# Optimization experiments

Measured on AMD Instinct MI355X. Metric: run time of the kernel, lower is better.

## Reference

```python
import jax, jax.numpy as jnp
import numpy as np

N = 100000
IN_CH = 500
H = 8           # heads
C1 = 8          # conv1 out_channels per head -> hidden 64
NCLS = 3        # conv2 out_channels (concat=False -> mean over heads)
NEG_SLOPE = 0.2


def _gatv2_layer(x, src, dst, Wl, Wr, att, bias, heads, ch, concat):
    n = x.shape[0]
    xl = (x @ Wl).reshape(n, heads, ch)   # source transform
    xr = (x @ Wr).reshape(n, heads, ch)   # target transform
    # per-edge attention logits: a^T LeakyReLU(xl[j] + xr[i])
    e = jax.nn.leaky_relu(xl[src] + xr[dst], NEG_SLOPE)   # [E,H,C]
    logits = jnp.einsum('ehc,hc->eh', e, att)             # [E,H]
    # segment softmax over edges sharing the same destination node
    m = jax.ops.segment_max(logits, dst, num_segments=n)  # [N,H]
    ex = jnp.exp(logits - m[dst])
    denom = jax.ops.segment_sum(ex, dst, num_segments=n)  # [N,H]
    alpha = ex / denom[dst]                               # [E,H]
    # scatter-add aggregation of source features weighted by attention
    out = jax.ops.segment_sum(alpha[:, :, None] * xl[src], dst, num_segments=n)  # [N,H,C]
    out = out.reshape(n, heads * ch) if concat else out.mean(axis=1)
    return out + bias


def _add_self_loops(edge_index, n):
    loop = jnp.arange(n, dtype=edge_index.dtype)
    src = jnp.concatenate([edge_index[0], loop])
    dst = jnp.concatenate([edge_index[1], loop])
    return src, dst


def setup_inputs() -> dict:
    key = jax.random.key(0)
    ks = jax.random.split(key, 10)
    E = 1600000
    x = jax.random.normal(ks[0], (N, IN_CH), dtype=jnp.float32)
    edge_index = jax.random.randint(ks[1], (2, E), 0, N, dtype=jnp.int64)
    s1 = 1.0 / np.sqrt(IN_CH)
    s2 = 1.0 / np.sqrt(H * C1)
    return {
        'x': x,
        'edge_index': edge_index,
        'W1l': jax.random.normal(ks[2], (IN_CH, H * C1), dtype=jnp.float32) * s1,
        'W1r': jax.random.normal(ks[3], (IN_CH, H * C1), dtype=jnp.float32) * s1,
        'att1': jax.random.normal(ks[4], (H, C1), dtype=jnp.float32) * 0.3,
        'b1': jnp.zeros((H * C1,), dtype=jnp.float32),
        'W2l': jax.random.normal(ks[5], (H * C1, H * NCLS), dtype=jnp.float32) * s2,
        'W2r': jax.random.normal(ks[6], (H * C1, H * NCLS), dtype=jnp.float32) * s2,
        'att2': jax.random.normal(ks[7], (H, NCLS), dtype=jnp.float32) * 0.3,
        'b2': jnp.zeros((NCLS,), dtype=jnp.float32),
    }


def reference(x, edge_index, W1l, W1r, att1, b1, W2l, W2r, att2, b2):
    # eval mode: dropout(p=0.6) is identity
    src, dst = _add_self_loops(edge_index, x.shape[0])
    h = _gatv2_layer(x, src, dst, W1l, W1r, att1, b1, H, C1, concat=True)
    h = jax.nn.elu(h)
    h = _gatv2_layer(h, src, dst, W2l, W2r, att2, b2, H, NCLS, concat=False)
    return jax.nn.softmax(h, axis=1)
```

## Files before the change

### kernel.cpp

```cpp
#include <hip/hip_runtime.h>
#include <cstdint>
#include <cstddef>

#define N_NODES 100000
#define E_EDGES 1600000
#define E_TOT   1700000
#define HEADS   8
#define C1      8
#define HC1     64
#define NCLS    3
#define HC2     24
#define IN_CH   500
#define NEG     0.2f

#define TILES   6250
#define NBLK    256

#define NPB     391
#define NBUCK   256
#define CHUNK   4096
#define NCHUNK  416
#define SCAP    8192

typedef __attribute__((ext_vector_type(8))) _Float16 f16x8;
typedef __attribute__((ext_vector_type(4))) _Float16 f16x4;
typedef __attribute__((ext_vector_type(4))) float f32x4;

__device__ __forceinline__ int edge_at(const int* __restrict__ ei, int idx, int mode) {
  return mode ? ei[idx] : ei[2 * idx];
}

__device__ __forceinline__ int detect_mode(const int* __restrict__ ei,
                                           int tid, int* shflag) {
  if (tid == 0) *shflag = 0;
  __syncthreads();
  int nz = 0;
#pragma unroll
  for (int i = 0; i < 16; ++i) nz |= ei[2 * (i * 256 + tid) + 1];
  if (__ballot(nz != 0)) {
    if ((tid & 63) == 0) atomicOr(shflag, 1);
  }
  __syncthreads();
  return *shflag;
}


__global__ __launch_bounds__(256) void k_cntA(const int* __restrict__ ei,
    int* __restrict__ cmat, const float* __restrict__ W1l,
    const float* __restrict__ W1r, _Float16* __restrict__ Wimg) {
  __shared__ int cnt[NBUCK];
  __shared__ int shflag;
  const int tid = threadIdx.x;

  if (blockIdx.x >= NCHUNK) {
    int b2 = blockIdx.x - NCHUNK;
    int t = b2 * 256 + tid;
    int col = t >> 9, k = t & 511;
    float v = 0.f;
    if (k < IN_CH) v = (col < HC1) ? W1l[k * HC1 + col] : W1r[k * HC1 + (col - HC1)];
    int boff = (col * 1024 + k * 2) ^ ((col & 7) << 4);
    Wimg[boff >> 1] = (_Float16)v;
    return;
  }

  const int mode = detect_mode(ei, tid, &shflag);
  const int e0 = blockIdx.x * CHUNK;
  cnt[tid] = 0;
  __syncthreads();
#pragma unroll
  for (int i = 0; i < 16; ++i) {
    int e = e0 + i * 256 + tid;
    if (e < E_TOT) {
      int d = (e < E_EDGES) ? edge_at(ei, E_EDGES + e, mode) : (e - E_EDGES);
      atomicAdd(&cnt[d / NPB], 1);
    }
  }
  __syncthreads();
  cmat[blockIdx.x * NBUCK + tid] = cnt[tid];
}

__global__ void k_scanA(int* __restrict__ cmat, int* __restrict__ bbase,
                        int* __restrict__ rowptr) {
  __shared__ int sh[NBUCK];
  int b = threadIdx.x;
  int run = 0;
  for (int c = 0; c < NCHUNK; ++c) {
    int v = cmat[c * NBUCK + b];
    cmat[c * NBUCK + b] = run;
    run += v;
  }
  int tot = run;
  sh[b] = tot;
  __syncthreads();
  for (int off = 1; off < NBUCK; off <<= 1) {
    int add = (b >= off) ? sh[b - off] : 0;
    __syncthreads();
    sh[b] += add;
    __syncthreads();
  }
  bbase[b] = sh[b] - tot;
  if (b == NBUCK - 1) {
    bbase[NBUCK] = sh[b];
    rowptr[N_NODES] = sh[b];
  }
}

__global__ __launch_bounds__(256) void k_grpA(const int* __restrict__ ei,
    const int* __restrict__ cmat, const int* __restrict__ bbase,
    unsigned* __restrict__ bstage) {
  __shared__ int cnt[NBUCK], ofs[NBUCK], cur[NBUCK], gbase[NBUCK];
  __shared__ unsigned buf[CHUNK];
  __shared__ int shflag;
  const int tid = threadIdx.x;
  const int e0 = blockIdx.x * CHUNK;
  const int mode = detect_mode(ei, tid, &shflag);
  cnt[tid] = 0;
  __syncthreads();

  unsigned pk[16]; int bk[16];
#pragma unroll
  for (int i = 0; i < 16; ++i) {
    int e = e0 + i * 256 + tid;
    bk[i] = -1;
    if (e < E_TOT) {
      int s, d;
      if (e < E_EDGES) { s = edge_at(ei, e, mode); d = edge_at(ei, E_EDGES + e, mode); }
      else             { s = e - E_EDGES; d = s; }
      int b = d / NPB;
      bk[i] = b;
      pk[i] = ((unsigned)s << 9) | (unsigned)(d - b * NPB);
      atomicAdd(&cnt[b], 1);
    }
  }
  __syncthreads();
  ofs[tid] = cnt[tid];
  __syncthreads();
  for (int off = 1; off < NBUCK; off <<= 1) {
    int add = (tid >= off) ? ofs[tid - off] : 0;
    __syncthreads();
    ofs[tid] += add;
    __syncthreads();
  }
  ofs[tid] -= cnt[tid];
  cur[tid] = ofs[tid];
  gbase[tid] = bbase[tid] + cmat[blockIdx.x * NBUCK + tid];
  __syncthreads();
#pragma unroll
  for (int i = 0; i < 16; ++i) {
    if (bk[i] >= 0) {
      int slot = atomicAdd(&cur[bk[i]], 1);
      buf[slot] = pk[i];
    }
  }
  __syncthreads();
  const int n = cnt[tid], s0 = ofs[tid], g = gbase[tid];
  for (int j = 0; j < n; ++j) {
    int gp = g + j;
    if ((unsigned)gp < (unsigned)E_TOT) bstage[gp] = buf[s0 + j];
  }
}

__global__ __launch_bounds__(256) void k_partB(const unsigned* __restrict__ bstage,
    const int* __restrict__ bbase, int* __restrict__ rowptr, int* __restrict__ esrc) {
  __shared__ unsigned edges[SCAP];
  __shared__ int lhist[NPB + 1];
  __shared__ int lptr[NPB];
  __shared__ int sh[256];
  const int b = blockIdx.x;
  const int tid = threadIdx.x;
  const int base = bbase[b];
  const int n = min(bbase[b + 1] - base, SCAP);
  const int nl = min(NPB, N_NODES - b * NPB);

  for (int k = tid; k < NPB; k += 256) lhist[k] = 0;
  for (int i = tid; i < n; i += 256) edges[i] = bstage[base + i];
  __syncthreads();
  for (int i = tid; i < n; i += 256) atomicAdd(&lhist[(int)(edges[i] & 511u)], 1);
  __syncthreads();
  int i0 = tid * 2;
  int v0 = (i0 < nl) ? lhist[i0] : 0;
  int v1 = (i0 + 1 < nl) ? lhist[i0 + 1] : 0;
  int tsum = v0 + v1;
  sh[tid] = tsum;
  __syncthreads();
  for (int off = 1; off < 256; off <<= 1) {
    int add = (tid >= off) ? sh[tid - off] : 0;
    __syncthreads();
    sh[tid] += add;
    __syncthreads();
  }
  int run = base + sh[tid] - tsum;
  if (i0 < nl)     lptr[i0] = run;
  if (i0 + 1 < nl) lptr[i0 + 1] = run + v0;
  __syncthreads();
  for (int k = tid; k < nl; k += 256) rowptr[b * NPB + k] = lptr[k];
  __syncthreads();
  for (int i = tid; i < n; i += 256) {
    unsigned pkv = edges[i];
    int pos = atomicAdd(&lptr[(int)(pkv & 511u)], 1);
    if ((unsigned)pos < (unsigned)E_TOT) esrc[pos] = (int)(pkv >> 9);
  }
}

#define ALO   16384
#define PBASE 32768

__global__ __launch_bounds__(512, 1) void k_gemm1(const float* __restrict__ x,
    const _Float16* __restrict__ Wimg, _Float16* __restrict__ xlh,
    float* __restrict__ xr) {
  __shared__ char lds[40960];
  const int tid  = threadIdx.x;
  const int lane = tid & 63, wid = tid >> 6;
  const int lrow = lane & 15, kg = lane >> 4;
  const int colgrp = wid & 3;
  const int kw0 = (wid >> 2) * 8;

  f16x8 bf[2][8];
#pragma unroll
  for (int n = 0; n < 2; ++n) {
    int col = colgrp * 32 + n * 16 + lrow;
#pragma unroll
    for (int kw = 0; kw < 8; ++kw) {
      int koff = (kw0 + kw) * 64 + kg * 16;
      int bo = (col * 1024 + koff) ^ ((col & 7) << 4);
      bf[n][kw] = *(const f16x8*)((const char*)Wimg + bo);
    }
  }

  int xoff[4], aoff[4], mode[4];
#pragma unroll
  for (int i = 0; i < 4; ++i) {
    int s = tid + i * 512;
    if (s < 2000) {
      int row = s / 125, c4 = s - row * 125;
      xoff[i] = row * 500 + c4 * 4;
      aoff[i] = (row * 1024 + c4 * 8) ^ ((row & 7) << 4);
      mode[i] = 0;
    } else {
      int p = s - 2000;
      int row = p / 3, j = p - row * 3;
      aoff[i] = (row * 1024 + 1000 + j * 8) ^ ((row & 7) << 4);
      xoff[i] = 0;
      mode[i] = 1;
    }
  }

  float4 rv[4];
  auto loadregs = [&](int tile) {
#pragma unroll
    for (int i = 0; i < 4; ++i)
      if (mode[i] == 0)
        rv[i] = *(const float4*)&x[(size_t)tile * 8000 + xoff[i]];
  };

  loadregs(blockIdx.x);

  for (int tile = blockIdx.x; tile < TILES; tile += NBLK) {
#pragma unroll
    for (int i = 0; i < 4; ++i) {
      f16x4 h, l;
      if (mode[i] == 0) {
        float vals[4] = {rv[i].x, rv[i].y, rv[i].z, rv[i].w};
#pragma unroll
        for (int c = 0; c < 4; ++c) {
          _Float16 hh = (_Float16)vals[c];
          float r = vals[c] - (float)hh;
          h[c] = hh;
          l[c] = (_Float16)(r * 2048.f);
        }
      } else {
        h = (f16x4){0, 0, 0, 0}; l = (f16x4){0, 0, 0, 0};
      }
      *(f16x4*)(lds + aoff[i]) = h;
      *(f16x4*)(lds + ALO + aoff[i]) = l;
    }
    __syncthreads();
    if (tile + NBLK < TILES) loadregs(tile + NBLK);

    f32x4 acch[2], accl[2];
    acch[0] = (f32x4){0,0,0,0}; acch[1] = (f32x4){0,0,0,0};
    accl[0] = (f32x4){0,0,0,0}; accl[1] = (f32x4){0,0,0,0};
#pragma unroll
    for (int kw = 0; kw < 8; ++kw) {
      const int koff = (kw0 + kw) * 64 + kg * 16;
      int ao = (lrow * 1024 + koff) ^ ((lrow & 7) << 4);
      f16x8 ah = *(const f16x8*)(lds + ao);
      f16x8 al = *(const f16x8*)(lds + ALO + ao);
#pragma unroll
      for (int n = 0; n < 2; ++n) {
        acch[n] = __builtin_amdgcn_mfma_f32_16x16x32_f16(ah, bf[n][kw], acch[n], 0, 0, 0);
        accl[n] = __builtin_amdgcn_mfma_f32_16x16x32_f16(al, bf[n][kw], accl[n], 0, 0, 0);
      }
    }
    float v[2][4];
#pragma unroll
    for (int n = 0; n < 2; ++n)
#pragma unroll
      for (int j = 0; j < 4; ++j)
        v[n][j] = acch[n][j] + accl[n][j] * 4.8828125e-4f;

    if (wid >= 4) {
      char* p = lds + PBASE + ((wid - 4) * 64 + lane) * 32;
      *(float4*)p       = make_float4(v[0][0], v[0][1], v[0][2], v[0][3]);
      *(float4*)(p+16)  = make_float4(v[1][0], v[1][1], v[1][2], v[1][3]);
    }
    __syncthreads();
    if (wid < 4) {
      const char* p = lds + PBASE + (wid * 64 + lane) * 32;
      float4 p0 = *(const float4*)p, p1 = *(const float4*)(p+16);
      v[0][0]+=p0.x; v[0][1]+=p0.y; v[0][2]+=p0.z; v[0][3]+=p0.w;
      v[1][0]+=p1.x; v[1][1]+=p1.y; v[1][2]+=p1.z; v[1][3]+=p1.w;
      const int bm0 = tile * 16;
      if (colgrp < 2) {
#pragma unroll
        for (int n = 0; n < 2; ++n) {
          int cc = colgrp * 32 + n * 16 + lrow;
#pragma unroll
          for (int j = 0; j < 4; ++j)
            xlh[(size_t)(bm0 + kg * 4 + j) * HC1 + cc] = (_Float16)v[n][j];
        }
      } else {
#pragma unroll
        for (int n = 0; n < 2; ++n) {
          int cc = (colgrp - 2) * 32 + n * 16 + lrow;
#pragma unroll
          for (int j = 0; j < 4; ++j)
            xr[(size_t)(bm0 + kg * 4 + j) * HC1 + cc] = v[n][j];
        }
      }
    }
  }
}

__global__ __launch_bounds__(256) void k_edge1(const _Float16* __restrict__ xl1h,
    const float* __restrict__ xr1, const float* __restrict__ att1,
    const float* __restrict__ b1, const int* __restrict__ rowptr,
    const int* __restrict__ esrc, _Float16* __restrict__ hbufh) {
  int t = blockIdx.x * blockDim.x + threadIdx.x;
  int node = t >> 3, h = t & 7;
  const float4* xrp = (const float4*)(xr1 + (size_t)node * HC1 + h * C1);
  float4 xa = xrp[0], xb = xrp[1];
  float xrv[8] = {xa.x, xa.y, xa.z, xa.w, xb.x, xb.y, xb.z, xb.w};
  const float4* ap = (const float4*)(att1 + h * C1);
  float4 aa = ap[0], ab = ap[1];
  float av[8] = {aa.x, aa.y, aa.z, aa.w, ab.x, ab.y, ab.z, ab.w};

  float m = -INFINITY, s = 0.f;
  float acc[8];
#pragma unroll
  for (int c = 0; c < 8; ++c) acc[c] = 0.f;

  auto gather = [&](int sn, float* v) {
    f16x8 q = *(const f16x8*)(xl1h + (size_t)sn * HC1 + h * C1);
#pragma unroll
    for (int c = 0; c < 8; ++c) v[c] = (float)q[c];
  };
  auto process = [&](const float* v) {
    float logit = 0.f;
#pragma unroll
    for (int c = 0; c < 8; ++c) {
      float u = v[c] + xrv[c];
      u = (u > 0.f) ? u : NEG * u;
      logit = fmaf(u, av[c], logit);
    }
    float mn = fmaxf(m, logit);
    float so = __expf(m - mn);
    float p  = __expf(logit - mn);
    s = s * so + p;
#pragma unroll
    for (int c = 0; c < 8; ++c) acc[c] = fmaf(acc[c], so, p * v[c]);
    m = mn;
  };

  int beg = rowptr[node], end = rowptr[node + 1];
  int i = beg;
  for (; i + 1 < end; i += 2) {
    int sn0 = esrc[i], sn1 = esrc[i + 1];
    if ((unsigned)sn0 >= N_NODES) sn0 = node;
    if ((unsigned)sn1 >= N_NODES) sn1 = node;
    float v0[8], v1[8];
    gather(sn0, v0); gather(sn1, v1);
    process(v0); process(v1);
  }
  if (i < end) {
    int sn0 = esrc[i];
    if ((unsigned)sn0 >= N_NODES) sn0 = node;
    float v0[8]; gather(sn0, v0); process(v0);
  }

  float inv = (s > 0.f) ? 1.f / s : 0.f;
  f16x8 ho;
#pragma unroll
  for (int c = 0; c < 8; ++c) {
    float v = fmaf(acc[c], inv, b1[h * C1 + c]);
    v = (v > 0.f) ? v : expm1f(v);
    ho[c] = (_Float16)v;
  }
  *(f16x8*)(hbufh + (size_t)node * HC1 + h * C1) = ho;
}

__global__ __launch_bounds__(256) void k_gemm2(const _Float16* __restrict__ hbufh,
    const float* __restrict__ W2l, const float* __restrict__ W2r,
    _Float16* __restrict__ xl2p, float* __restrict__ xr2) {
  __shared__ float w[64][48];
  int tid = threadIdx.x;
  for (int i = tid; i < 64 * 48; i += 256) {
    int k = i / 48, j = i - k * 48;
    w[k][j] = (j < HC2) ? W2l[k * HC2 + j] : W2r[k * HC2 + (j - HC2)];
  }
  __syncthreads();
  int node = blockIdx.x * 256 + tid;
  if (node >= N_NODES) return;
  float acc[48];
#pragma unroll
  for (int j = 0; j < 48; ++j) acc[j] = 0.f;
  const f16x8* hp = (const f16x8*)(hbufh + (size_t)node * HC1);
  for (int k0 = 0; k0 < 64; k0 += 16) {
    float rv[16];
    f16x8 ra = hp[k0 / 8], rb = hp[k0 / 8 + 1];
#pragma unroll
    for (int j = 0; j < 8; ++j) { rv[j] = (float)ra[j]; rv[8 + j] = (float)rb[j]; }
#pragma unroll
    for (int kk = 0; kk < 16; ++kk) {
      float hv = rv[kk];
      const float4* wrow = (const float4*)&w[k0 + kk][0];
#pragma unroll
      for (int j4 = 0; j4 < 12; ++j4) {
        float4 wv = wrow[j4];
        acc[j4*4+0] = fmaf(hv, wv.x, acc[j4*4+0]);
        acc[j4*4+1] = fmaf(hv, wv.y, acc[j4*4+1]);
        acc[j4*4+2] = fmaf(hv, wv.z, acc[j4*4+2]);
        acc[j4*4+3] = fmaf(hv, wv.w, acc[j4*4+3]);
      }
    }
  }
  f16x8 hx[4];
#pragma unroll
  for (int q = 0; q < 4; ++q) {
#pragma unroll
    for (int hh = 0; hh < 2; ++hh) {
      int hd = q * 2 + hh;
#pragma unroll
      for (int c = 0; c < 4; ++c)
        hx[q][hh * 4 + c] = (c < 3) ? (_Float16)acc[hd * 3 + c] : (_Float16)0.f;
    }
    *(f16x8*)(xl2p + (size_t)node * 32 + q * 8) = hx[q];
  }
  float4* rp = (float4*)(xr2 + (size_t)node * HC2);
#pragma unroll
  for (int j4 = 0; j4 < 6; ++j4)
    rp[j4] = make_float4(acc[24+j4*4+0], acc[24+j4*4+1], acc[24+j4*4+2], acc[24+j4*4+3]);
}

__global__ __launch_bounds__(256) void k_edge2(const _Float16* __restrict__ xl2p,
    const float* __restrict__ xr2, const float* __restrict__ att2,
    const float* __restrict__ b2, const int* __restrict__ rowptr,
    const int* __restrict__ esrc, float* __restrict__ out) {
  int t = blockIdx.x * blockDim.x + threadIdx.x;
  int node = t >> 3, h = t & 7;
  float xrv[3], av[3];
#pragma unroll
  for (int c = 0; c < 3; ++c) {
    xrv[c] = xr2[(size_t)node * HC2 + h * NCLS + c];
    av[c]  = att2[h * NCLS + c];
  }
  float m = -INFINITY, s = 0.f;
  float acc[3] = {0.f, 0.f, 0.f};

  auto process = [&](const float* v) {
    float logit = 0.f;
#pragma unroll
    for (int c = 0; c < 3; ++c) {
      float u = v[c] + xrv[c];
      u = (u > 0.f) ? u : NEG * u;
      logit = fmaf(u, av[c], logit);
    }
    float mn = fmaxf(m, logit);
    float so = __expf(m - mn);
    float p  = __expf(logit - mn);
    s = s * so + p;
#pragma unroll
    for (int c = 0; c < 3; ++c) acc[c] = fmaf(acc[c], so, p * v[c]);
    m = mn;
  };

  int beg = rowptr[node], end = rowptr[node + 1];
  int i = beg;
  for (; i + 1 < end; i += 2) {
    int sn0 = esrc[i], sn1 = esrc[i + 1];
    if ((unsigned)sn0 >= N_NODES) sn0 = node;
    if ((unsigned)sn1 >= N_NODES) sn1 = node;
    f16x4 q0 = *(const f16x4*)(xl2p + (size_t)sn0 * 32 + h * 4);
    f16x4 q1 = *(const f16x4*)(xl2p + (size_t)sn1 * 32 + h * 4);
    float v0[3] = {(float)q0[0], (float)q0[1], (float)q0[2]};
    float v1[3] = {(float)q1[0], (float)q1[1], (float)q1[2]};
    process(v0); process(v1);
  }
  if (i < end) {
    int sn0 = esrc[i];
    if ((unsigned)sn0 >= N_NODES) sn0 = node;
    f16x4 q0 = *(const f16x4*)(xl2p + (size_t)sn0 * 32 + h * 4);
    float v0[3] = {(float)q0[0], (float)q0[1], (float)q0[2]};
    process(v0);
  }

  float inv = (s > 0.f) ? 1.f / s : 0.f;
  float o[3];
#pragma unroll
  for (int c = 0; c < 3; ++c) o[c] = acc[c] * inv;
#pragma unroll
  for (int off = 1; off < 8; off <<= 1) {
#pragma unroll
    for (int c = 0; c < 3; ++c) o[c] += __shfl_xor(o[c], off);
  }
  if (h < 3) {
    float z[3];
#pragma unroll
    for (int c = 0; c < 3; ++c) z[c] = o[c] * 0.125f + b2[c];
    float mx = fmaxf(fmaxf(z[0], z[1]), z[2]);
    float e0 = __expf(z[0] - mx), e1 = __expf(z[1] - mx), e2 = __expf(z[2] - mx);
    float sum = e0 + e1 + e2;
    float num = (h == 0) ? e0 : (h == 1) ? e1 : e2;
    out[(size_t)node * NCLS + h] = num / sum;
  }
}

extern "C" void kernel_launch(void* const* d_in, const int* in_sizes, int n_in,
                              void* d_out, int out_size, void* d_ws, size_t ws_size,
                              hipStream_t stream) {
  (void)in_sizes; (void)n_in; (void)out_size; (void)ws_size;
  const float* x    = (const float*)d_in[0];
  const int*   ei   = (const int*)d_in[1];
  const float* W1l  = (const float*)d_in[2];
  const float* W1r  = (const float*)d_in[3];
  const float* att1 = (const float*)d_in[4];
  const float* b1   = (const float*)d_in[5];
  const float* W2l  = (const float*)d_in[6];
  const float* W2r  = (const float*)d_in[7];
  const float* att2 = (const float*)d_in[8];
  const float* b2   = (const float*)d_in[9];
  float* out = (float*)d_out;

  char* w = (char*)d_ws;
  _Float16* xl1h  = (_Float16*)(w);
  float* xr1      = (float*)(w + 12800000);
  _Float16* hbufh = (_Float16*)(w + 38400000);
  _Float16* Wimg  = (_Float16*)(w + 64000000);
  _Float16* xl2p  = (_Float16*)(w);
  float* xr2      = (float*)(w + 6400000);
  unsigned* bstage = (unsigned*)(w);
  char* ip = w + 76800000;
  int* rowptr = (int*)(ip);
  int* cmat   = (int*)(ip + 400128);
  int* bbase  = (int*)(ip + 826112);
  int* esrc   = (int*)(ip + 827648);

  k_cntA   <<<NCHUNK + 256, 256, 0, stream>>>(ei, cmat, W1l, W1r, Wimg);
  k_scanA  <<<1, NBUCK, 0, stream>>>(cmat, bbase, rowptr);
  k_grpA   <<<NCHUNK, 256, 0, stream>>>(ei, cmat, bbase, bstage);
  k_partB  <<<NBUCK, 256, 0, stream>>>(bstage, bbase, rowptr, esrc);
  k_gemm1  <<<NBLK, 512, 0, stream>>>(x, Wimg, xl1h, xr1);
  k_edge1  <<<(N_NODES * HEADS) / 256, 256, 0, stream>>>(xl1h, xr1, att1, b1, rowptr, esrc, hbufh);
  k_gemm2  <<<(N_NODES + 255) / 256, 256, 0, stream>>>(hbufh, W2l, W2r, xl2p, xr2);
  k_edge2  <<<(N_NODES * HEADS) / 256, 256, 0, stream>>>(xl2p, xr2, att2, b2, rowptr, esrc, out);
}
```

Measured before the change: 229.0 us.

## Fuse layer-2 projection GEMM into layer-1 edge aggregation kernel

Merges the second-layer linear transform into the first-layer edge-softmax/aggregation kernel. Each block of 32 nodes writes its ELU hidden rows into shared memory, then multiplies them by W2l and W2r held in LDS and writes xl2p and xr2 directly. This removes one kernel launch and the global write and re-read of the hidden buffer. In exchange it adds about 29 KB of shared memory per block, which may lower occupancy of the gather-heavy edge kernel, and relies on the f16x4 type being defined.

Result: faster. 219.6 us, median of 2 (-4.1%).

```diff
diff --git a/kernel.cpp b/kernel.cpp
--- a/kernel.cpp
+++ b/kernel.cpp
@@ -332,11 +332,23 @@
   }
 }
 
-__global__ __launch_bounds__(256) void k_edge1(const _Float16* __restrict__ xl1h,
+__global__ __launch_bounds__(256) void k_edge1g2(const _Float16* __restrict__ xl1h,
     const float* __restrict__ xr1, const float* __restrict__ att1,
-    const float* __restrict__ b1, const int* __restrict__ rowptr,
-    const int* __restrict__ esrc, _Float16* __restrict__ hbufh) {
-  int t = blockIdx.x * blockDim.x + threadIdx.x;
+    const float* __restrict__ b1, const float* __restrict__ W2l,
+    const float* __restrict__ W2r, const int* __restrict__ rowptr,
+    const int* __restrict__ esrc, _Float16* __restrict__ xl2p,
+    float* __restrict__ xr2) {
+  __shared__ float w[64][48];
+  __shared__ float hsh[32][65];
+  __shared__ float out48[32][49];
+  const int tid = threadIdx.x;
+
+  for (int i = tid; i < 64 * 48; i += 256) {
+    int k = i / 48, j = i - k * 48;
+    w[k][j] = (j < HC2) ? W2l[k * HC2 + j] : W2r[k * HC2 + (j - HC2)];
+  }
+
+  int t = blockIdx.x * 256 + tid;
   int node = t >> 3, h = t & 7;
   const float4* xrp = (const float4*)(xr1 + (size_t)node * HC1 + h * C1);
   float4 xa = xrp[0], xb = xrp[1];
@@ -389,67 +401,37 @@
   }
 
   float inv = (s > 0.f) ? 1.f / s : 0.f;
-  f16x8 ho;
+  const int ln = tid >> 3;
 #pragma unroll
   for (int c = 0; c < 8; ++c) {
     float v = fmaf(acc[c], inv, b1[h * C1 + c]);
     v = (v > 0.f) ? v : expm1f(v);
-    ho[c] = (_Float16)v;
-  }
-  *(f16x8*)(hbufh + (size_t)node * HC1 + h * C1) = ho;
-}
-
-__global__ __launch_bounds__(256) void k_gemm2(const _Float16* __restrict__ hbufh,
-    const float* __restrict__ W2l, const float* __restrict__ W2r,
-    _Float16* __restrict__ xl2p, float* __restrict__ xr2) {
-  __shared__ float w[64][48];
-  int tid = threadIdx.x;
-  for (int i = tid; i < 64 * 48; i += 256) {
-    int k = i / 48, j = i - k * 48;
-    w[k][j] = (j < HC2) ? W2l[k * HC2 + j] : W2r[k * HC2 + (j - HC2)];
-  }
-  __syncthreads();
-  int node = blockIdx.x * 256 + tid;
-  if (node >= N_NODES) return;
-  float acc[48];
-#pragma unroll
-  for (int j = 0; j < 48; ++j) acc[j] = 0.f;
-  const f16x8* hp = (const f16x8*)(hbufh + (size_t)node * HC1);
-  for (int k0 = 0; k0 < 64; k0 += 16) {
-    float rv[16];
-    f16x8 ra = hp[k0 / 8], rb = hp[k0 / 8 + 1];
-#pragma unroll
-    for (int j = 0; j < 8; ++j) { rv[j] = (float)ra[j]; rv[8 + j] = (float)rb[j]; }
-#pragma unroll
-    for (int kk = 0; kk < 16; ++kk) {
-      float hv = rv[kk];
-      const float4* wrow = (const float4*)&w[k0 + kk][0];
-#pragma unroll
-      for (int j4 = 0; j4 < 12; ++j4) {
-        float4 wv = wrow[j4];
-        acc[j4*4+0] = fmaf(hv, wv.x, acc[j4*4+0]);
-        acc[j4*4+1] = fmaf(hv, wv.y, acc[j4*4+1]);
-        acc[j4*4+2] = fmaf(hv, wv.z, acc[j4*4+2]);
-        acc[j4*4+3] = fmaf(hv, wv.w, acc[j4*4+3]);
-      }
-    }
-  }
-  f16x8 hx[4];
-#pragma unroll
-  for (int q = 0; q < 4; ++q) {
-#pragma unroll
-    for (int hh = 0; hh < 2; ++hh) {
-      int hd = q * 2 + hh;
-#pragma unroll
-      for (int c = 0; c < 4; ++c)
-        hx[q][hh * 4 + c] = (c < 3) ? (_Float16)acc[hd * 3 + c] : (_Float16)0.f;
-    }
-    *(f16x8*)(xl2p + (size_t)node * 32 + q * 8) = hx[q];
-  }
-  float4* rp = (float4*)(xr2 + (size_t)node * HC2);
-#pragma unroll
-  for (int j4 = 0; j4 < 6; ++j4)
-    rp[j4] = make_float4(acc[24+j4*4+0], acc[24+j4*4+1], acc[24+j4*4+2], acc[24+j4*4+3]);
+    hsh[ln][h * 8 + c] = v;
+  }
+  __syncthreads();
+
+  const int g = tid & 7;
+  float a6[6] = {0.f, 0.f, 0.f, 0.f, 0.f, 0.f};
+#pragma unroll 4
+  for (int k = 0; k < 64; ++k) {
+    float hv = hsh[ln][k];
+    const float* wr = &w[k][g * 6];
+#pragma unroll
+    for (int j = 0; j < 6; ++j) a6[j] = fmaf(hv, wr[j], a6[j]);
+  }
+#pragma unroll
+  for (int j = 0; j < 6; ++j) out48[ln][g * 6 + j] = a6[j];
+  __syncthreads();
+
+  const int gnode = blockIdx.x * 32 + ln;
+  f16x4 hx;
+#pragma unroll
+  for (int c = 0; c < 3; ++c) hx[c] = (_Float16)out48[ln][h * 3 + c];
+  hx[3] = (_Float16)0.f;
+  *(f16x4*)(xl2p + (size_t)gnode * 32 + h * 4) = hx;
+#pragma unroll
+  for (int c = 0; c < 3; ++c)
+    xr2[(size_t)gnode * HC2 + h * 3 + c] = out48[ln][24 + h * 3 + c];
 }
 
 __global__ __launch_bounds__(256) void k_edge2(const _Float16* __restrict__ xl2p,
@@ -544,10 +526,9 @@
   char* w = (char*)d_ws;
   _Float16* xl1h  = (_Float16*)(w);
   float* xr1      = (float*)(w + 12800000);
-  _Float16* hbufh = (_Float16*)(w + 38400000);
+  _Float16* xl2p  = (_Float16*)(w + 38400000);
+  float* xr2      = (float*)(w + 44800000);
   _Float16* Wimg  = (_Float16*)(w + 64000000);
-  _Float16* xl2p  = (_Float16*)(w);
-  float* xr2      = (float*)(w + 6400000);
   unsigned* bstage = (unsigned*)(w);
   char* ip = w + 76800000;
   int* rowptr = (int*)(ip);
@@ -555,12 +536,12 @@
   int* bbase  = (int*)(ip + 826112);
   int* esrc   = (int*)(ip + 827648);
 
-  k_cntA   <<<NCHUNK + 256, 256, 0, stream>>>(ei, cmat, W1l, W1r, Wimg);
-  k_scanA  <<<1, NBUCK, 0, stream>>>(cmat, bbase, rowptr);
-  k_grpA   <<<NCHUNK, 256, 0, stream>>>(ei, cmat, bbase, bstage);
-  k_partB  <<<NBUCK, 256, 0, stream>>>(bstage, bbase, rowptr, esrc);
-  k_gemm1  <<<NBLK, 512, 0, stream>>>(x, Wimg, xl1h, xr1);
-  k_edge1  <<<(N_NODES * HEADS) / 256, 256, 0, stream>>>(xl1h, xr1, att1, b1, rowptr, esrc, hbufh);
-  k_gemm2  <<<(N_NODES + 255) / 256, 256, 0, stream>>>(hbufh, W2l, W2r, xl2p, xr2);
-  k_edge2  <<<(N_NODES * HEADS) / 256, 256, 0, stream>>>(xl2p, xr2, att2, b2, rowptr, esrc, out);
-}
+  k_cntA    <<<NCHUNK + 256, 256, 0, stream>>>(ei, cmat, W1l, W1r, Wimg);
+  k_scanA   <<<1, NBUCK, 0, stream>>>(cmat, bbase, rowptr);
+  k_grpA    <<<NCHUNK, 256, 0, stream>>>(ei, cmat, bbase, bstage);
+  k_partB   <<<NBUCK, 256, 0, stream>>>(bstage, bbase, rowptr, esrc);
+  k_gemm1   <<<NBLK, 512, 0, stream>>>(x, Wimg, xl1h, xr1);
+  k_edge1g2 <<<N_NODES / 32, 256, 0, stream>>>(xl1h, xr1, att1, b1, W2l, W2r,
+                                               rowptr, esrc, xl2p, xr2);
+  k_edge2   <<<(N_NODES * HEADS) / 256, 256, 0, stream>>>(xl2p, xr2, att2, b2, rowptr, esrc, out);
+}
```
